# Kernel optimization log

Measured on AMD Instinct MI355X. Metric: run time of the kernel, lower is better.

## Reference

```python
import jax, jax.numpy as jnp
import numpy as np

N = 100000
E = 1600000
D_IN = 64
D_OUT = 64
LN_EPS = 1e-5


def setup_inputs() -> dict:
    key = jax.random.key(0)
    k1, k2, k3 = jax.random.split(key, 3)
    x = jax.random.normal(k1, (N, D_IN), dtype=jnp.float32)
    edge_index = jax.random.randint(k2, (2, E), 0, N, dtype=jnp.int64)
    # nn.Linear(in_dim*2, out_dim): weight [out, 2*in], bias [out]
    W = jax.random.normal(k3, (D_OUT, 2 * D_IN), dtype=jnp.float32) * (1.0 / np.sqrt(2 * D_IN))
    b = jnp.zeros((D_OUT,), dtype=jnp.float32)
    gamma = jnp.ones((D_OUT,), dtype=jnp.float32)
    beta = jnp.zeros((D_OUT,), dtype=jnp.float32)
    return {"x": x, "edge_index": edge_index, "W": W, "b": b, "gamma": gamma, "beta": beta}


def reference(x, edge_index, W, b, gamma, beta):
    i, j = edge_index[0], edge_index[1]          # dst, src
    msg = x[j]                                    # [E, D] gather of source features
    agg = jax.ops.segment_sum(msg, i, num_segments=N)                      # [N, D]
    deg = jax.ops.segment_sum(jnp.ones((E,), x.dtype), i, num_segments=N)  # [N]
    agg = agg / jnp.maximum(deg, 1.0)[:, None]    # mean aggregation
    h = jnp.concatenate([x, agg], axis=-1)        # [N, 2D]
    out = jax.nn.relu(h @ W.T + b)                # [N, D_OUT]
    # LayerNorm over last dim (dropout p=0 -> identity)
    mu = jnp.mean(out, axis=-1, keepdims=True)
    var = jnp.var(out, axis=-1, keepdims=True)
    return (out - mu) * jax.lax.rsqrt(var + LN_EPS) * gamma + beta
```

## Files before the change

kernel.cpp:

```cpp
#include <hip/hip_runtime.h>

#define LN_EPS 1e-5f
#define SBSH   14
#define NSB    7
#define CAP1   268288
#define CPS    131
#define BN     128
#define BC     2368
#define NBK    782
#define CSTRIDE 8
#define ASTR   72

typedef __attribute__((ext_vector_type(8))) short short8;
typedef __attribute__((ext_vector_type(8))) unsigned short ushort8;
typedef __attribute__((ext_vector_type(4))) float v4f;

__device__ __forceinline__ unsigned short f2bf(float f) {
    union { float f; unsigned u; } v; v.f = f;
    unsigned r = (v.u + 0x7fffu + ((v.u >> 16) & 1u)) >> 16;
    return (unsigned short)r;
}
__device__ __forceinline__ float bf2f(unsigned short h) {
    union { unsigned u; float f; } v; v.u = ((unsigned)h) << 16;
    return v.f;
}

__global__ __launch_bounds__(256) void bin1_kernel(
    const int* __restrict__ ei, int* __restrict__ cursor1,
    int* __restrict__ pairs1, const float* __restrict__ W,
    unsigned short* __restrict__ WTB, const float4* __restrict__ x4,
    ushort4* __restrict__ xb4, int E, int N)
{
    __shared__ int h[64];
    __shared__ int hbase[64];
    int t = threadIdx.x;
    int cp = t & 7;

    if (blockIdx.x == 0) {
        for (int i = t; i < 8192; i += 256) {
            int j = i & 7, l = (i >> 3) & 63, st = i >> 9;
            int s = st >> 2, tt = st & 3;
            WTB[i] = f2bf(W[(tt * 16 + (l & 15)) * 128 + s * 32 + (l >> 4) * 8 + j]);
        }
    }
    {
        int total4 = N * 16;
        for (int i = blockIdx.x * 256 + t; i < total4; i += gridDim.x * 256) {
            float4 v = x4[i];
            ushort4 u;
            u.x = f2bf(v.x); u.y = f2bf(v.y); u.z = f2bf(v.z); u.w = f2bf(v.w);
            xb4[i] = u;
        }
    }

    for (int i = t; i < 64; i += 256) h[i] = 0;
    __syncthreads();
    int e0 = blockIdx.x * 4096;
    int dstA[16], srcA[16], rkA[16];
    #pragma unroll
    for (int i = 0; i < 16; ++i) {
        int e = e0 + i * 256 + t;
        int dst = 0, src = 0, rk = -1;
        if (e < E) {
            dst = ei[e]; src = ei[E + e];
            if ((unsigned)dst < (unsigned)N) {
                rk = atomicAdd(&h[cp * 8 + (dst >> SBSH)], 1);
                if ((unsigned)src >= (unsigned)N) src = 0;
            } else { dst = 0; }
        }
        dstA[i] = dst; srcA[i] = src; rkA[i] = rk;
    }
    __syncthreads();
    if (t < 8) {
        int tot = 0;
        #pragma unroll
        for (int c = 0; c < 8; ++c) tot += h[c * 8 + t];
        int gb = tot ? atomicAdd(&cursor1[t * 16], tot) : 0;
        int run = gb;
        #pragma unroll
        for (int c = 0; c < 8; ++c) { hbase[c * 8 + t] = run; run += h[c * 8 + t]; }
    }
    __syncthreads();
    #pragma unroll
    for (int i = 0; i < 16; ++i) {
        if (rkA[i] >= 0) {
            int sb = dstA[i] >> SBSH;
            int slot = hbase[cp * 8 + sb] + rkA[i];
            if (slot < CAP1)
                pairs1[(size_t)sb * CAP1 + slot] = ((dstA[i] & 16383) << 17) | srcA[i];
        }
    }
}

__global__ __launch_bounds__(256) void bin2_kernel(
    const int* __restrict__ cursor1, const int* __restrict__ pairs1,
    int* __restrict__ cursor2, int* __restrict__ pairs2)
{
    __shared__ int h[128], hbase[128];
    int t = threadIdx.x;
    int sb = blockIdx.x / CPS;
    int off0 = (blockIdx.x % CPS) * 2048;
    int tot = cursor1[sb * 16]; if (tot > CAP1) tot = CAP1;
    int m = tot - off0;
    if (m <= 0) return;
    if (m > 2048) m = 2048;
    if (t < 128) h[t] = 0;
    __syncthreads();
    const int* p1 = pairs1 + (size_t)sb * CAP1 + off0;
    int pvA[8], rkA[8];
    #pragma unroll
    for (int i = 0; i < 8; ++i) {
        int idx = i * 256 + t;
        int pv = 0, rk = -1;
        if (idx < m) { pv = p1[idx]; rk = atomicAdd(&h[(pv >> 24) & 127], 1); }
        pvA[i] = pv; rkA[i] = rk;
    }
    __syncthreads();
    if (t < 128) {
        int c = h[t];
        hbase[t] = c ? atomicAdd(&cursor2[(sb * 128 + t) * CSTRIDE], c) : 0;
    }
    __syncthreads();
    #pragma unroll
    for (int i = 0; i < 8; ++i) {
        if (rkA[i] >= 0) {
            int bl = (pvA[i] >> 24) & 127;
            int g = sb * 128 + bl;
            int slot = hbase[bl] + rkA[i];
            if (g < NBK && slot < BC)
                pairs2[(size_t)g * BC + slot] = pvA[i] & 0xFFFFFF;
        }
    }
}

__global__ __launch_bounds__(1024, 8) void sortgather_kernel(
    const int* __restrict__ cursor2, const int* __restrict__ pairs2,
    const unsigned short* __restrict__ xb, const unsigned short* __restrict__ WTB,
    const float* __restrict__ b, const float* __restrict__ gamma,
    const float* __restrict__ beta, float* __restrict__ out, int N)
{
    __shared__ int srcS[BC];
    __shared__ int cnt[BN], off[BN];
    __shared__ __align__(16) unsigned short aggS[BN * ASTR];
    int t = threadIdx.x;
    int g = blockIdx.x;
    int bsize = cursor2[g * CSTRIDE]; if (bsize > BC) bsize = BC;
    const int* pb = pairs2 + (size_t)g * BC;

    if (t < BN) cnt[t] = 0;
    __syncthreads();
    int pvA[3], rkA[3];
    #pragma unroll
    for (int i = 0; i < 3; ++i) {
        int idx = i * 1024 + t;
        int pv = 0, rk = -1;
        if (idx < bsize) { pv = pb[idx]; rk = atomicAdd(&cnt[(pv >> 17) & 127], 1); }
        pvA[i] = pv; rkA[i] = rk;
    }
    __syncthreads();
    if (t < 64) {
        int c0 = cnt[t], c1 = cnt[t + 64];
        int v0 = c0, v1 = c1;
        #pragma unroll
        for (int d = 1; d < 64; d <<= 1) {
            int u0 = __shfl_up(v0, d);
            int u1 = __shfl_up(v1, d);
            if (t >= d) { v0 += u0; v1 += u1; }
        }
        int tot0 = __shfl(v0, 63);
        off[t]      = v0 - c0;
        off[t + 64] = v1 - c1 + tot0;
    }
    __syncthreads();
    #pragma unroll
    for (int i = 0; i < 3; ++i) {
        if (rkA[i] >= 0) {
            int bl = (pvA[i] >> 17) & 127;
            srcS[off[bl] + rkA[i]] = pvA[i] & 0x1FFFF;
        }
    }
    __syncthreads();

    int lane = t & 63, wv = t >> 6;
    int g8 = lane >> 3, f8 = lane & 7;
    int ln = wv * 8 + g8;
    int deg = cnt[ln], base = off[ln];

    int wm = deg;
    wm = max(wm, __shfl_xor(wm, 8));
    wm = max(wm, __shfl_xor(wm, 16));
    wm = max(wm, __shfl_xor(wm, 32));
    int cl = (deg > 0) ? deg - 1 : 0;

    float acc[8];
    #pragma unroll
    for (int k = 0; k < 8; ++k) acc[k] = 0.f;

    const unsigned short* xf = xb + (size_t)f8 * 8;

    for (int j = 0; j < wm; j += 8) {
        short8 a[8];
        #pragma unroll
        for (int k = 0; k < 8; ++k) {
            int jj = j + k; if (jj > cl) jj = cl;
            int s = srcS[base + jj];
            if (s >= N) s = 0;
            a[k] = *(const short8*)(xf + (size_t)s * 64);
        }
        #pragma unroll
        for (int k = 0; k < 8; ++k) {
            float m = (j + k < deg) ? 1.f : 0.f;
            #pragma unroll
            for (int e = 0; e < 8; ++e)
                acc[e] = fmaf(m, bf2f((unsigned short)a[k][e]), acc[e]);
        }
    }

    {
        float inv = 1.0f / fmaxf((float)deg, 1.0f);
        ushort8 r;
        #pragma unroll
        for (int k = 0; k < 8; ++k) r[k] = f2bf(acc[k] * inv);
        *(ushort8*)(aggS + ln * ASTR + f8 * 8) = r;
    }
    __syncthreads();

    if (wv < 8) {
        int c = lane & 15, q = lane >> 4;
        int nb = g * BN + wv * 16;
        int nm = nb + c; if (nm >= N) nm = N - 1;
        int lnl = wv * 16 + c;

        const short8* WB = (const short8*)WTB;
        v4f acc4[4];
        #pragma unroll
        for (int tt = 0; tt < 4; ++tt) acc4[tt] = 0.f;

        #pragma unroll
        for (int s = 0; s < 2; ++s) {
            short8 af = *(const short8*)(xb + (size_t)nm * 64 + s * 32 + q * 8);
            #pragma unroll
            for (int tt = 0; tt < 4; ++tt)
                acc4[tt] = __builtin_amdgcn_mfma_f32_16x16x32_bf16(
                    af, WB[(s * 4 + tt) * 64 + lane], acc4[tt], 0, 0, 0);
        }
        #pragma unroll
        for (int s = 0; s < 2; ++s) {
            short8 af = *(const short8*)(aggS + lnl * ASTR + s * 32 + q * 8);
            #pragma unroll
            for (int tt = 0; tt < 4; ++tt)
                acc4[tt] = __builtin_amdgcn_mfma_f32_16x16x32_bf16(
                    af, WB[((2 + s) * 4 + tt) * 64 + lane], acc4[tt], 0, 0, 0);
        }

        float bb[4], gg[4], be[4];
        #pragma unroll
        for (int tt = 0; tt < 4; ++tt) {
            bb[tt] = b[tt * 16 + c];
            gg[tt] = gamma[tt * 16 + c];
            be[tt] = beta[tt * 16 + c];
        }
        #pragma unroll
        for (int r = 0; r < 4; ++r) {
            int node = nb + q * 4 + r;
            float v[4]; float s0 = 0.f, q0 = 0.f;
            #pragma unroll
            for (int tt = 0; tt < 4; ++tt) {
                float vv = acc4[tt][r] + bb[tt];
                vv = fmaxf(vv, 0.f);
                v[tt] = vv; s0 += vv; q0 += vv * vv;
            }
            #pragma unroll
            for (int o = 1; o <= 8; o <<= 1) {
                s0 += __shfl_xor(s0, o);
                q0 += __shfl_xor(q0, o);
            }
            float mu  = s0 * (1.0f / 64.0f);
            float var = q0 * (1.0f / 64.0f) - mu * mu;
            float rs  = rsqrtf(var + LN_EPS);
            if (node < N) {
                #pragma unroll
                for (int tt = 0; tt < 4; ++tt)
                    out[(size_t)node * 64 + tt * 16 + c] = (v[tt] - mu) * rs * gg[tt] + be[tt];
            }
        }
    }
}

extern "C" void kernel_launch(void* const* d_in, const int* in_sizes, int n_in,
                              void* d_out, int out_size, void* d_ws, size_t ws_size,
                              hipStream_t stream)
{
    const float* x     = (const float*)d_in[0];
    const int*   ei    = (const int*)d_in[1];
    const float* W     = (const float*)d_in[2];
    const float* b     = (const float*)d_in[3];
    const float* gamma = (const float*)d_in[4];
    const float* beta  = (const float*)d_in[5];

    int N = in_sizes[0] / 64;
    int E = in_sizes[1] / 2;

    int* wsI = (int*)d_ws;
    int* cursor1 = wsI;
    int* cursor2 = wsI + 128;
    unsigned short* WTB = (unsigned short*)(wsI + 128 + 896 * CSTRIDE);
    int* pairs2 = wsI + 128 + 896 * CSTRIDE + 4096;
    unsigned short* xb = (unsigned short*)(pairs2 + (size_t)NBK * BC);

    int* pairs1 = (int*)d_out;
    float* out = (float*)d_out;

    hipMemsetAsync(cursor1, 0, (size_t)(128 + 896 * CSTRIDE) * sizeof(int), stream);

    int b1 = (E + 4095) / 4096;
    bin1_kernel<<<b1, 256, 0, stream>>>(ei, cursor1, pairs1, W, WTB,
                                        (const float4*)x, (ushort4*)xb, E, N);

    bin2_kernel<<<NSB * CPS, 256, 0, stream>>>(cursor1, pairs1, cursor2, pairs2);

    sortgather_kernel<<<NBK, 1024, 0, stream>>>(cursor2, pairs2, xb, WTB,
                                                b, gamma, beta, out, N);
}
```

Measured before the change: 164.1 us.

## Pad per-node edge lists to multiples of four and software-pipeline gathers

Each node's source list in shared memory is padded to a multiple of four. Padding slots point to a new zero row appended after the bf16 feature table, so masking and index clamping are no longer needed. The gather loop now reads four indices with one vector LDS load and double-buffers the row loads, issuing the next four while the previous four are accumulated. Each lane's loop runs to its own padded degree rather than the wave-wide max of 8-step chunks. This costs a larger shared array, a fill pass over it, and a write to the element after the row-major bf16 buffer, which must have room for it.

```diff
diff --git a/kernel.cpp b/kernel.cpp
--- a/kernel.cpp
+++ b/kernel.cpp
@@ -7,6 +7,7 @@
 #define CPS    131
 #define BN     128
 #define BC     2368
+#define SCAP   2752
 #define NBK    782
 #define CSTRIDE 8
 #define ASTR   72
@@ -41,6 +42,10 @@
             int j = i & 7, l = (i >> 3) & 63, st = i >> 9;
             int s = st >> 2, tt = st & 3;
             WTB[i] = f2bf(W[(tt * 16 + (l & 15)) * 128 + s * 32 + (l >> 4) * 8 + j]);
+        }
+        if (t < 16) {
+            ushort4 z; z.x = 0; z.y = 0; z.z = 0; z.w = 0;
+            xb4[(size_t)N * 16 + t] = z;
         }
     }
     {
@@ -139,7 +144,7 @@
     const float* __restrict__ b, const float* __restrict__ gamma,
     const float* __restrict__ beta, float* __restrict__ out, int N)
 {
-    __shared__ int srcS[BC];
+    __shared__ __align__(16) int srcS[SCAP];
     __shared__ int cnt[BN], off[BN];
     __shared__ __align__(16) unsigned short aggS[BN * ASTR];
     int t = threadIdx.x;
@@ -148,6 +153,7 @@
     const int* pb = pairs2 + (size_t)g * BC;
 
     if (t < BN) cnt[t] = 0;
+    for (int i = t; i < SCAP; i += 1024) srcS[i] = N;
     __syncthreads();
     int pvA[3], rkA[3];
     #pragma unroll
@@ -159,7 +165,7 @@
     }
     __syncthreads();
     if (t < 64) {
-        int c0 = cnt[t], c1 = cnt[t + 64];
+        int c0 = (cnt[t] + 3) & ~3, c1 = (cnt[t + 64] + 3) & ~3;
         int v0 = c0, v1 = c1;
         #pragma unroll
         for (int d = 1; d < 64; d <<= 1) {
@@ -185,12 +191,7 @@
     int g8 = lane >> 3, f8 = lane & 7;
     int ln = wv * 8 + g8;
     int deg = cnt[ln], base = off[ln];
-
-    int wm = deg;
-    wm = max(wm, __shfl_xor(wm, 8));
-    wm = max(wm, __shfl_xor(wm, 16));
-    wm = max(wm, __shfl_xor(wm, 32));
-    int cl = (deg > 0) ? deg - 1 : 0;
+    int pdeg = (deg + 3) & ~3;
 
     float acc[8];
     #pragma unroll
@@ -198,22 +199,39 @@
 
     const unsigned short* xf = xb + (size_t)f8 * 8;
 
-    for (int j = 0; j < wm; j += 8) {
-        short8 a[8];
-        #pragma unroll
-        for (int k = 0; k < 8; ++k) {
-            int jj = j + k; if (jj > cl) jj = cl;
-            int s = srcS[base + jj];
-            if (s >= N) s = 0;
-            a[k] = *(const short8*)(xf + (size_t)s * 64);
-        }
-        #pragma unroll
-        for (int k = 0; k < 8; ++k) {
-            float m = (j + k < deg) ? 1.f : 0.f;
-            #pragma unroll
-            for (int e = 0; e < 8; ++e)
-                acc[e] = fmaf(m, bf2f((unsigned short)a[k][e]), acc[e]);
-        }
+    short8 A0, A1, A2, A3;
+    if (pdeg > 0) {
+        int4 ix = *(const int4*)(srcS + base);
+        A0 = *(const short8*)(xf + (size_t)ix.x * 64);
+        A1 = *(const short8*)(xf + (size_t)ix.y * 64);
+        A2 = *(const short8*)(xf + (size_t)ix.z * 64);
+        A3 = *(const short8*)(xf + (size_t)ix.w * 64);
+    }
+    for (int j = 4; j < pdeg; j += 4) {
+        int4 ix = *(const int4*)(srcS + base + j);
+        short8 B0 = *(const short8*)(xf + (size_t)ix.x * 64);
+        short8 B1 = *(const short8*)(xf + (size_t)ix.y * 64);
+        short8 B2 = *(const short8*)(xf + (size_t)ix.z * 64);
+        short8 B3 = *(const short8*)(xf + (size_t)ix.w * 64);
+        #pragma unroll
+        for (int e = 0; e < 8; ++e) acc[e] += bf2f((unsigned short)A0[e]);
+        #pragma unroll
+        for (int e = 0; e < 8; ++e) acc[e] += bf2f((unsigned short)A1[e]);
+        #pragma unroll
+        for (int e = 0; e < 8; ++e) acc[e] += bf2f((unsigned short)A2[e]);
+        #pragma unroll
+        for (int e = 0; e < 8; ++e) acc[e] += bf2f((unsigned short)A3[e]);
+        A0 = B0; A1 = B1; A2 = B2; A3 = B3;
+    }
+    if (pdeg > 0) {
+        #pragma unroll
+        for (int e = 0; e < 8; ++e) acc[e] += bf2f((unsigned short)A0[e]);
+        #pragma unroll
+        for (int e = 0; e < 8; ++e) acc[e] += bf2f((unsigned short)A1[e]);
+        #pragma unroll
+        for (int e = 0; e < 8; ++e) acc[e] += bf2f((unsigned short)A2[e]);
+        #pragma unroll
+        for (int e = 0; e < 8; ++e) acc[e] += bf2f((unsigned short)A3[e]);
     }
 
     {
```

New measurement: 172.1 us. 4.9% more time.
